# Performance work log

Measured on AMD Instinct MI355X. Metric: run time of the kernel, lower is better.

The kernel has to match this reference:

```python
import jax, jax.numpy as jnp
import numpy as np

B, D, N_CLASSES = 8192, 256, 512
ALPHA = 0.1


def setup_inputs() -> dict:
    key = jax.random.key(0)
    k1, k2 = jax.random.split(key)
    y_pred = jax.random.normal(k1, (B, D), dtype=jnp.float32)
    y_true = jax.random.randint(k2, (B, 1), 0, N_CLASSES, dtype=jnp.int32)
    return {"y_true": y_true, "y_pred": y_pred}


def reference(y_true, y_pred):
    # L2-normalize each embedding row; tf.math.divide_no_nan -> 0 when norm == 0
    norm = jnp.sqrt(jnp.sum(jnp.square(y_pred), axis=-1, keepdims=True))  # [B,1]
    z = jnp.where(norm > 0, y_pred / norm, 0.0)  # [B,D]
    # All-pairs cosine similarity (source's 'cos' metric returns the dot product)
    sims = jnp.einsum("id,jd->ij", z, z)  # [B,B]
    labels = y_true.reshape(-1)  # [B]
    equal = labels[:, None] == labels[None, :]  # [B,B] bool
    eq_f = equal.astype(sims.dtype)
    n_pos = jnp.sum(eq_f)
    n_neg = jnp.asarray(B * B, sims.dtype) - n_pos
    positive_dist = jnp.sum(sims * eq_f) / n_pos
    negative_dist = jnp.sum(sims * (1.0 - eq_f)) / n_neg
    return jnp.maximum(positive_dist - negative_dist + ALPHA, 0.0)
```

## Files before the change

### kernel.cpp

```cpp
#include <hip/hip_runtime.h>
#include <math.h>

#define B 8192
#define D 256
#define NCLS 512
#define ALPHA 0.1f

__global__ __launch_bounds__(256) void k_class(const int* __restrict__ labels,
                                               const float* __restrict__ y_pred,
                                               float* __restrict__ s,
                                               int* __restrict__ cnt_out)
{
    __shared__ int   list[B];
    __shared__ int   cnt;
    __shared__ float accs[4][D];

    const int c    = blockIdx.x;
    const int tid  = threadIdx.x;
    const int wave = tid >> 6;
    const int lane = tid & 63;

    if (tid == 0) cnt = 0;
    __syncthreads();

    const int4* l4 = (const int4*)labels;
    for (int k = tid; k < B / 4; k += 256) {
        int4 v = l4[k];
        if (v.x == c) list[atomicAdd(&cnt, 1)] = 4 * k + 0;
        if (v.y == c) list[atomicAdd(&cnt, 1)] = 4 * k + 1;
        if (v.z == c) list[atomicAdd(&cnt, 1)] = 4 * k + 2;
        if (v.w == c) list[atomicAdd(&cnt, 1)] = 4 * k + 3;
    }
    __syncthreads();
    const int n = cnt;

    float4 acc = make_float4(0.f, 0.f, 0.f, 0.f);
    for (int j = wave; j < n; j += 4) {
        const int i = list[j];
        const float4* row = (const float4*)(y_pred + (size_t)i * D);
        float4 v = row[lane];
        float sq = v.x * v.x + v.y * v.y + v.z * v.z + v.w * v.w;
#pragma unroll
        for (int off = 32; off; off >>= 1) sq += __shfl_xor(sq, off, 64);
        const float inv = (sq > 0.f) ? (1.0f / sqrtf(sq)) : 0.f;
        acc.x += v.x * inv; acc.y += v.y * inv;
        acc.z += v.z * inv; acc.w += v.w * inv;
    }
    ((float4*)accs[wave])[lane] = acc;
    __syncthreads();

    const float sum = accs[0][tid] + accs[1][tid] + accs[2][tid] + accs[3][tid];
    s[(size_t)c * D + tid] = sum;
    if (tid == 0) cnt_out[c] = n;
}

__global__ __launch_bounds__(1024) void k_final(const float* __restrict__ s,
                                                const int* __restrict__ cnt,
                                                float* __restrict__ out)
{
    __shared__ float tpart[4][D];
    __shared__ float redsq[16];
    __shared__ float redall[4];
    __shared__ float rednp[4];

    const int tid = threadIdx.x;
    const int g = tid >> 8;
    const int d = tid & 255;

    float tl = 0.f, sq = 0.f;
#pragma unroll 4
    for (int c = g; c < NCLS; c += 4) {
        const float v = s[(size_t)c * D + d];
        tl += v;
        sq += v * v;
    }
    tpart[g][d] = tl;
#pragma unroll
    for (int off = 32; off; off >>= 1) sq += __shfl_xor(sq, off, 64);
    if ((tid & 63) == 0) redsq[tid >> 6] = sq;
    __syncthreads();

    float sall = 0.f, np = 0.f;
    if (g == 0) {
        const float t_d = tpart[0][d] + tpart[1][d] + tpart[2][d] + tpart[3][d];
        sall = t_d * t_d;
        const float c0 = (float)cnt[d];
        const float c1 = (float)cnt[d + 256];
        np = c0 * c0 + c1 * c1;
#pragma unroll
        for (int off = 32; off; off >>= 1) {
            sall += __shfl_xor(sall, off, 64);
            np   += __shfl_xor(np,   off, 64);
        }
        if ((d & 63) == 0) { redall[d >> 6] = sall; rednp[d >> 6] = np; }
    }
    __syncthreads();

    if (tid == 0) {
        float s_pos = 0.f;
#pragma unroll
        for (int i = 0; i < 16; ++i) s_pos += redsq[i];
        const float s_all = redall[0] + redall[1] + redall[2] + redall[3];
        const float np_   = rednp[0] + rednp[1] + rednp[2] + rednp[3];
        const float nn    = (float)B * (float)B - np_;
        const float pd    = s_pos / np_;
        const float nd    = (s_all - s_pos) / nn;
        const float r     = pd - nd + ALPHA;
        *out = (r > 0.f) ? r : 0.f;
    }
}

extern "C" void kernel_launch(void* const* d_in, const int* in_sizes, int n_in,
                              void* d_out, int out_size, void* d_ws, size_t ws_size,
                              hipStream_t stream) {
    const int*   y_true = (const int*)d_in[0];
    const float* y_pred = (const float*)d_in[1];
    float* out = (float*)d_out;

    char* ws = (char*)d_ws;
    float* s   = (float*)(ws);
    int*   cnt = (int*)(ws + (size_t)NCLS * D * sizeof(float));

    k_class<<<NCLS, 256, 0, stream>>>(y_true, y_pred, s, cnt);
    k_final<<<1, 1024, 0, stream>>>(s, cnt, out);
}
```

Before: 80.39 us.

## Fuse class-sum and final reduction into one cooperative kernel with grid syncs

Merges the per-class normalized-sum kernel and the single-block final reduction into one cooperative kernel separated by grid-wide syncs. The final reduction is spread across 257 blocks (one per feature dimension plus one for counts) instead of one block, and the row-gather loop is unrolled by two to keep more loads in flight. This removes a second kernel launch and the serial single-block tail, at the cost of cooperative-launch overhead and two grid barriers. All 512 blocks must be co-resident, which the per-block LDS use of about 36KB has to allow.

```diff
diff --git a/kernel.cpp b/kernel.cpp
--- a/kernel.cpp
+++ b/kernel.cpp
@@ -1,112 +1,136 @@
 #include <hip/hip_runtime.h>
+#include <hip/hip_cooperative_groups.h>
 #include <math.h>
+
+namespace cg = cooperative_groups;
 
 #define B 8192
 #define D 256
 #define NCLS 512
 #define ALPHA 0.1f
 
-__global__ __launch_bounds__(256) void k_class(const int* __restrict__ labels,
-                                               const float* __restrict__ y_pred,
-                                               float* __restrict__ s,
-                                               int* __restrict__ cnt_out)
+__global__ __launch_bounds__(256) void k_fused(
+        const int* __restrict__ labels,
+        const float* __restrict__ y_pred,
+        float* __restrict__ s,
+        int* __restrict__ cnt_g,
+        float2* __restrict__ part,
+        float* __restrict__ nposp,
+        float* __restrict__ out)
 {
     __shared__ int   list[B];
-    __shared__ int   cnt;
+    __shared__ int   cnt_s;
     __shared__ float accs[4][D];
+    __shared__ float red[2][4];
 
     const int c    = blockIdx.x;
     const int tid  = threadIdx.x;
     const int wave = tid >> 6;
     const int lane = tid & 63;
 
-    if (tid == 0) cnt = 0;
+    if (tid == 0) cnt_s = 0;
     __syncthreads();
 
     const int4* l4 = (const int4*)labels;
     for (int k = tid; k < B / 4; k += 256) {
         int4 v = l4[k];
-        if (v.x == c) list[atomicAdd(&cnt, 1)] = 4 * k + 0;
-        if (v.y == c) list[atomicAdd(&cnt, 1)] = 4 * k + 1;
-        if (v.z == c) list[atomicAdd(&cnt, 1)] = 4 * k + 2;
-        if (v.w == c) list[atomicAdd(&cnt, 1)] = 4 * k + 3;
+        if (v.x == c) list[atomicAdd(&cnt_s, 1)] = 4 * k + 0;
+        if (v.y == c) list[atomicAdd(&cnt_s, 1)] = 4 * k + 1;
+        if (v.z == c) list[atomicAdd(&cnt_s, 1)] = 4 * k + 2;
+        if (v.w == c) list[atomicAdd(&cnt_s, 1)] = 4 * k + 3;
     }
     __syncthreads();
-    const int n = cnt;
+    const int n = cnt_s;
 
     float4 acc = make_float4(0.f, 0.f, 0.f, 0.f);
-    for (int j = wave; j < n; j += 4) {
-        const int i = list[j];
-        const float4* row = (const float4*)(y_pred + (size_t)i * D);
-        float4 v = row[lane];
-        float sq = v.x * v.x + v.y * v.y + v.z * v.z + v.w * v.w;
+    int j0 = wave, j1 = wave + 4;
+    for (; j1 < n; j0 += 8, j1 += 8) {
+        const float4 v0 = ((const float4*)(y_pred + (size_t)list[j0] * D))[lane];
+        const float4 v1 = ((const float4*)(y_pred + (size_t)list[j1] * D))[lane];
+        float q0 = v0.x * v0.x + v0.y * v0.y + v0.z * v0.z + v0.w * v0.w;
+        float q1 = v1.x * v1.x + v1.y * v1.y + v1.z * v1.z + v1.w * v1.w;
 #pragma unroll
-        for (int off = 32; off; off >>= 1) sq += __shfl_xor(sq, off, 64);
-        const float inv = (sq > 0.f) ? (1.0f / sqrtf(sq)) : 0.f;
-        acc.x += v.x * inv; acc.y += v.y * inv;
-        acc.z += v.z * inv; acc.w += v.w * inv;
+        for (int off = 32; off; off >>= 1) {
+            q0 += __shfl_xor(q0, off, 64);
+            q1 += __shfl_xor(q1, off, 64);
+        }
+        const float i0 = (q0 > 0.f) ? (1.0f / sqrtf(q0)) : 0.f;
+        const float i1 = (q1 > 0.f) ? (1.0f / sqrtf(q1)) : 0.f;
+        acc.x += v0.x * i0 + v1.x * i1;
+        acc.y += v0.y * i0 + v1.y * i1;
+        acc.z += v0.z * i0 + v1.z * i1;
+        acc.w += v0.w * i0 + v1.w * i1;
+    }
+    if (j0 < n) {
+        const float4 v0 = ((const float4*)(y_pred + (size_t)list[j0] * D))[lane];
+        float q0 = v0.x * v0.x + v0.y * v0.y + v0.z * v0.z + v0.w * v0.w;
+#pragma unroll
+        for (int off = 32; off; off >>= 1) q0 += __shfl_xor(q0, off, 64);
+        const float i0 = (q0 > 0.f) ? (1.0f / sqrtf(q0)) : 0.f;
+        acc.x += v0.x * i0; acc.y += v0.y * i0;
+        acc.z += v0.z * i0; acc.w += v0.w * i0;
     }
     ((float4*)accs[wave])[lane] = acc;
     __syncthreads();
 
-    const float sum = accs[0][tid] + accs[1][tid] + accs[2][tid] + accs[3][tid];
-    s[(size_t)c * D + tid] = sum;
-    if (tid == 0) cnt_out[c] = n;
-}
+    s[(size_t)c * D + tid] = accs[0][tid] + accs[1][tid] + accs[2][tid] + accs[3][tid];
+    if (tid == 0) cnt_g[c] = n;
 
-__global__ __launch_bounds__(1024) void k_final(const float* __restrict__ s,
-                                                const int* __restrict__ cnt,
-                                                float* __restrict__ out)
-{
-    __shared__ float tpart[4][D];
-    __shared__ float redsq[16];
-    __shared__ float redall[4];
-    __shared__ float rednp[4];
+    __threadfence();
+    cg::this_grid().sync();
 
-    const int tid = threadIdx.x;
-    const int g = tid >> 8;
-    const int d = tid & 255;
+    if (c < D) {
+        const int d = c;
+        const float v0 = s[(size_t)tid * D + d];
+        const float v1 = s[(size_t)(tid + 256) * D + d];
+        float t  = v0 + v1;
+        float sq = v0 * v0 + v1 * v1;
+#pragma unroll
+        for (int off = 32; off; off >>= 1) {
+            t  += __shfl_xor(t,  off, 64);
+            sq += __shfl_xor(sq, off, 64);
+        }
+        if (lane == 0) { red[0][wave] = t; red[1][wave] = sq; }
+        __syncthreads();
+        if (tid == 0) {
+            const float td  = red[0][0] + red[0][1] + red[0][2] + red[0][3];
+            const float sqd = red[1][0] + red[1][1] + red[1][2] + red[1][3];
+            part[d] = make_float2(td * td, sqd);
+        }
+    } else if (c == D) {
+        const float n0 = (float)cnt_g[tid];
+        const float n1 = (float)cnt_g[tid + 256];
+        float np = n0 * n0 + n1 * n1;
+#pragma unroll
+        for (int off = 32; off; off >>= 1) np += __shfl_xor(np, off, 64);
+        if (lane == 0) red[0][wave] = np;
+        __syncthreads();
+        if (tid == 0) *nposp = red[0][0] + red[0][1] + red[0][2] + red[0][3];
+    }
 
-    float tl = 0.f, sq = 0.f;
-#pragma unroll 4
-    for (int c = g; c < NCLS; c += 4) {
-        const float v = s[(size_t)c * D + d];
-        tl += v;
-        sq += v * v;
-    }
-    tpart[g][d] = tl;
-#pragma unroll
-    for (int off = 32; off; off >>= 1) sq += __shfl_xor(sq, off, 64);
-    if ((tid & 63) == 0) redsq[tid >> 6] = sq;
-    __syncthreads();
+    __threadfence();
+    cg::this_grid().sync();
 
-    float sall = 0.f, np = 0.f;
-    if (g == 0) {
-        const float t_d = tpart[0][d] + tpart[1][d] + tpart[2][d] + tpart[3][d];
-        sall = t_d * t_d;
-        const float c0 = (float)cnt[d];
-        const float c1 = (float)cnt[d + 256];
-        np = c0 * c0 + c1 * c1;
+    if (c == 0) {
+        const float2 p = part[tid];
+        float sall = p.x, spos = p.y;
 #pragma unroll
         for (int off = 32; off; off >>= 1) {
             sall += __shfl_xor(sall, off, 64);
-            np   += __shfl_xor(np,   off, 64);
+            spos += __shfl_xor(spos, off, 64);
         }
-        if ((d & 63) == 0) { redall[d >> 6] = sall; rednp[d >> 6] = np; }
-    }
-    __syncthreads();
-
-    if (tid == 0) {
-        float s_pos = 0.f;
-#pragma unroll
-        for (int i = 0; i < 16; ++i) s_pos += redsq[i];
-        const float s_all = redall[0] + redall[1] + redall[2] + redall[3];
-        const float np_   = rednp[0] + rednp[1] + rednp[2] + rednp[3];
-        const float nn    = (float)B * (float)B - np_;
-        const float pd    = s_pos / np_;
-        const float nd    = (s_all - s_pos) / nn;
-        const float r     = pd - nd + ALPHA;
-        *out = (r > 0.f) ? r : 0.f;
+        if (lane == 0) { red[0][wave] = sall; red[1][wave] = spos; }
+        __syncthreads();
+        if (tid == 0) {
+            const float s_all = red[0][0] + red[0][1] + red[0][2] + red[0][3];
+            const float s_pos = red[1][0] + red[1][1] + red[1][2] + red[1][3];
+            const float np_   = *nposp;
+            const float nn    = (float)B * (float)B - np_;
+            const float pd    = s_pos / np_;
+            const float nd    = (s_all - s_pos) / nn;
+            const float r     = pd - nd + ALPHA;
+            *out = (r > 0.f) ? r : 0.f;
+        }
     }
 }
 
@@ -118,9 +142,12 @@
     float* out = (float*)d_out;
 
     char* ws = (char*)d_ws;
-    float* s   = (float*)(ws);
-    int*   cnt = (int*)(ws + (size_t)NCLS * D * sizeof(float));
+    float*  s     = (float*)(ws);
+    int*    cnt   = (int*)(ws + 524288);
+    float2* part  = (float2*)(ws + 526336);
+    float*  nposp = (float*)(ws + 528384);
 
-    k_class<<<NCLS, 256, 0, stream>>>(y_true, y_pred, s, cnt);
-    k_final<<<1, 1024, 0, stream>>>(s, cnt, out);
+    void* args[] = {&y_true, &y_pred, &s, &cnt, &part, &nposp, &out};
+    hipLaunchCooperativeKernel((const void*)k_fused, dim3(NCLS), dim3(256),
+                               args, 0, stream);
 }
```

Measured after the change: 232.2 us. +188.9%, slower.
